# Performance work log

Hardware: AMD Instinct MI355X
Metric: run time of the kernel (lower is better)

Reference implementation:

```python
import jax, jax.numpy as jnp
import numpy as np

EPS = 1e-5


def _conv1x1(w, x):
    # w: [O, C, 1, 1], x: [B, C, H, W] -> [B, O, H, W]
    return jnp.einsum('oc,bchw->bohw', w[:, :, 0, 0], x)


def _bn_train(y, g, b):
    # BatchNorm2d in training mode: batch statistics over (B, H, W)
    m = y.mean(axis=(0, 2, 3), keepdims=True)
    v = y.var(axis=(0, 2, 3), keepdims=True)
    return (y - m) * jax.lax.rsqrt(v + EPS) * g[None, :, None, None] + b[None, :, None, None]


def setup_inputs() -> dict:
    key = jax.random.key(0)
    ks = jax.random.split(key, 8)
    B, C, H, W = 16, 512, 32, 32
    width, heads, hd, out_ch = 128, 4, 32, 512  # out_chans*expansion = 512
    return {
        'x': jax.random.normal(ks[0], (B, C, H, W), jnp.float32),
        'conv1_w': jax.random.normal(ks[1], (width, C, 1, 1), jnp.float32) * 0.05,
        'bn1_g': jnp.ones((width,), jnp.float32),
        'bn1_b': jnp.zeros((width,), jnp.float32),
        'qkv_w': jax.random.normal(ks[2], (3 * width, width, 1, 1), jnp.float32) * 0.05,
        'rw': jax.random.normal(ks[3], (1, heads, hd, 1, W), jnp.float32),
        'rh': jax.random.normal(ks[4], (1, heads, hd, H, 1), jnp.float32),
        'conv2_w': jax.random.normal(ks[5], (out_ch, width, 1, 1), jnp.float32) * 0.05,
        'bn2_g': jnp.ones((out_ch,), jnp.float32),
        'bn2_b': jnp.zeros((out_ch,), jnp.float32),
    }


def reference(x, conv1_w, bn1_g, bn1_b, qkv_w, rw, rh, conv2_w, bn2_g, bn2_b):
    B, C, H, W = x.shape
    heads = rw.shape[1]
    width = qkv_w.shape[1]
    hd = width // heads
    scale = hd ** (-0.5)
    N = H * W

    identity = x
    # conv1 = BaseConv: 1x1 conv (no bias) + BN + ReLU
    y = jax.nn.relu(_bn_train(_conv1x1(conv1_w, x), bn1_g, bn1_b))

    # Attention with relative position bias
    qkv = _conv1x1(qkv_w, y)                       # [B, 3*width, H, W]
    qkv = qkv.reshape(B, 3, heads, hd, N)          # split channels as (3, heads, hd)
    q, k, v = qkv[:, 0], qkv[:, 1], qkv[:, 2]      # each [B, heads, hd, N]

    attn_content = jnp.einsum('bhdn,bhdm->bhnm', q, k) * scale  # [B, heads, N, N]
    r = (rw + rh).reshape(heads, hd, N)                          # [heads, hd, N]
    attn_position = jnp.einsum('bhdn,hdm->bhnm', q, r) * scale
    attn = jax.nn.softmax(attn_content + attn_position, axis=-1)
    out = jnp.einsum('bhnm,bhdm->bhdn', attn, v)   # [B, heads, hd, N]
    y = out.reshape(B, width, H, W)

    # conv2 + BN, residual add, ReLU (stride==1: no pooling, no down_sample)
    y = _bn_train(_conv1x1(conv2_w, y), bn2_g, bn2_b)
    y = y + identity
    return jax.nn.relu(y)
```

## Files before the change

### kernel.cpp

```cpp
#include <hip/hip_runtime.h>
#include <cstddef>
#include <cstdint>

constexpr int BATCH = 16;
constexpr int NQ    = 1024;
constexpr float QSCALE = 0.17677669529663687f * 1.4426950408889634f;

typedef __attribute__((ext_vector_type(8))) short bf8;
typedef __attribute__((ext_vector_type(4))) float f32x4;
typedef __attribute__((ext_vector_type(4))) unsigned short us4;
typedef __attribute__((ext_vector_type(8))) unsigned short us8;

__device__ inline unsigned short f2bf(float x) {
  union { float f; uint32_t u; } c{x};
  uint32_t r = c.u + 0x7fffu + ((c.u >> 16) & 1u);
  return (unsigned short)(r >> 16);
}
__device__ inline float b2f(unsigned short v) {
  union { uint32_t u; float f; } c{(uint32_t)v << 16};
  return c.f;
}
__device__ inline float fast_exp2(float x) {
#if __has_builtin(__builtin_amdgcn_exp2f)
  return __builtin_amdgcn_exp2f(x);
#else
  return exp2f(x);
#endif
}

__global__ __launch_bounds__(256) void k_wcvt(const float* __restrict__ w1,
                                              const float* __restrict__ wq,
                                              const float* __restrict__ w2,
                                              unsigned short* __restrict__ o1,
                                              unsigned short* __restrict__ oq,
                                              unsigned short* __restrict__ o2,
                                              float* __restrict__ S2,
                                              float* __restrict__ Q2) {
  if (blockIdx.x == 88) {
    const int t = threadIdx.x;
    S2[t * 2] = 0.f; S2[t * 2 + 1] = 0.f;
    Q2[t * 2] = 0.f; Q2[t * 2 + 1] = 0.f;
    return;
  }
  int idx = (blockIdx.x * 256 + threadIdx.x) * 8;
  const float* s; unsigned short* d; int off;
  if (idx < 65536)        { s = w1; d = o1; off = idx; }
  else if (idx < 114688)  { s = wq; d = oq; off = idx - 65536; }
  else                    { s = w2; d = o2; off = idx - 114688; }
  float4 a = *(const float4*)(s + off);
  float4 b = *(const float4*)(s + off + 4);
  us8 o = {f2bf(a.x), f2bf(a.y), f2bf(a.z), f2bf(a.w),
           f2bf(b.x), f2bf(b.y), f2bf(b.z), f2bf(b.w)};
  *(us8*)(d + off) = o;
}

__global__ __launch_bounds__(256) void k_conv1(const float* __restrict__ x,
                                               const unsigned short* __restrict__ W,
                                               unsigned short* __restrict__ y1T) {
  constexpr int BS = 68;
  __shared__ unsigned short Bl[64 * BS];

  const int bb = blockIdx.z;
  const int n0 = blockIdx.x * 64;
  const int tid = threadIdx.x, lane = tid & 63, wv = tid >> 6;
  const int wn = wv & 1, wm = wv >> 1;
  const int i = lane & 15, g = lane >> 4;

  const int kb = tid >> 4, nb = tid & 15;

  f32x4 acc[2][4];
#pragma unroll
  for (int a = 0; a < 2; ++a)
#pragma unroll
    for (int b = 0; b < 4; ++b) acc[a][b] = {0.f, 0.f, 0.f, 0.f};

  float4 rv[4];
#pragma unroll
  for (int r = 0; r < 4; ++r)
    rv[r] = *(const float4*)(x + (((size_t)(bb * 512 + kb * 4 + r)) << 10) + n0 + nb * 4);

  for (int s = 0; s < 8; ++s) {
    bf8 wf[4][2];
#pragma unroll
    for (int b = 0; b < 4; ++b)
#pragma unroll
      for (int h = 0; h < 2; ++h)
        wf[b][h] = *(const bf8*)(W + (size_t)(wm * 64 + b * 16 + i) * 512 + s * 64 + h * 32 + g * 8);

    __syncthreads();
#pragma unroll
    for (int j = 0; j < 4; ++j) {
      us4 pk = {f2bf((&rv[0].x)[j]), f2bf((&rv[1].x)[j]),
                f2bf((&rv[2].x)[j]), f2bf((&rv[3].x)[j])};
      *(us4*)&Bl[(nb * 4 + j) * BS + kb * 4] = pk;
    }
    __syncthreads();

    if (s < 7) {
#pragma unroll
      for (int r = 0; r < 4; ++r)
        rv[r] = *(const float4*)(x + (((size_t)(bb * 512 + (s + 1) * 64 + kb * 4 + r)) << 10) + n0 + nb * 4);
    }

#pragma unroll
    for (int h = 0; h < 2; ++h) {
      bf8 af[2];
#pragma unroll
      for (int a = 0; a < 2; ++a)
        af[a] = *(const bf8*)&Bl[(wn * 32 + a * 16 + i) * BS + h * 32 + g * 8];
#pragma unroll
      for (int a = 0; a < 2; ++a)
#pragma unroll
        for (int b = 0; b < 4; ++b)
          acc[a][b] = __builtin_amdgcn_mfma_f32_16x16x32_bf16(wf[b][h], af[a], acc[a][b], 0, 0, 0);
    }
  }

#pragma unroll
  for (int a = 0; a < 2; ++a)
#pragma unroll
    for (int b = 0; b < 4; ++b) {
      const int n = n0 + wn * 32 + a * 16 + i;
      const int c = wm * 64 + b * 16 + 4 * g;
      us4 pk = {f2bf(acc[a][b][0]), f2bf(acc[a][b][1]), f2bf(acc[a][b][2]), f2bf(acc[a][b][3])};
      *(us4*)(y1T + ((size_t)(bb << 10) + n) * 128 + c) = pk;
    }
}

template<int KTOT, int MODE>
__global__ __launch_bounds__(256) void k_mm(const unsigned short* __restrict__ W,
                                            const unsigned short* __restrict__ Bact,
                                            const float* __restrict__ scl,
                                            const float* __restrict__ sht,
                                            const float* __restrict__ rw,
                                            const float* __restrict__ rh,
                                            unsigned short* __restrict__ out0,
                                            unsigned short* __restrict__ out1,
                                            unsigned short* __restrict__ out2) {
  constexpr int BS = 136;
  __shared__ unsigned short Blds[128 * BS];
  __shared__ float scl_s[128], sht_s[128];

  const int bb = blockIdx.z, mt = blockIdx.y;
  const int n0 = blockIdx.x * 128, m0 = mt * 64;
  const int tid = threadIdx.x, lane = tid & 63, wv = tid >> 6;
  const int wn = wv & 1, wm = wv >> 1;
  const int i = lane & 15, g = lane >> 4;

  const unsigned short* Bp = Bact + ((size_t)bb * NQ + n0) * KTOT;

  f32x4 acc[4][2];
#pragma unroll
  for (int a = 0; a < 4; ++a)
#pragma unroll
    for (int b = 0; b < 2; ++b) acc[a][b] = {0.f, 0.f, 0.f, 0.f};

  const int sn = tid >> 1;
  const int sk = (tid & 1) * 8;

  if (tid < 128) { scl_s[tid] = scl[tid]; sht_s[tid] = sht[tid]; }
  bf8 wf[2][4];
#pragma unroll
  for (int b = 0; b < 2; ++b)
#pragma unroll
    for (int h = 0; h < 4; ++h)
      wf[b][h] = *(const bf8*)(W + (size_t)(m0 + wm * 32 + b * 16 + i) * 128 + h * 32 + g * 8);
  __syncthreads();
#pragma unroll
  for (int p = 0; p < 8; ++p) {
    us8 v = *(const us8*)(Bp + (size_t)sn * 128 + sk + p * 16);
    const int kb = sk + p * 16;
    float scv[8], shv[8];
    *(float4*)scv = *(const float4*)&scl_s[kb];
    *(float4*)(scv + 4) = *(const float4*)&scl_s[kb + 4];
    *(float4*)shv = *(const float4*)&sht_s[kb];
    *(float4*)(shv + 4) = *(const float4*)&sht_s[kb + 4];
#pragma unroll
    for (int j = 0; j < 8; ++j)
      v[j] = f2bf(fmaxf(fmaf(b2f(v[j]), scv[j], shv[j]), 0.f));
    *(us8*)(&Blds[sn * BS + sk + p * 16]) = v;
  }
  __syncthreads();

  const bool actA = (mt >= 4);
  if (actA) {
#pragma unroll
    for (int h = 0; h < 4; ++h) {
      bf8 af[4];
#pragma unroll
      for (int a = 0; a < 4; ++a)
        af[a] = *(const bf8*)&Blds[(wn * 64 + a * 16 + i) * BS + h * 32 + g * 8];
#pragma unroll
      for (int a = 0; a < 4; ++a)
#pragma unroll
        for (int b = 0; b < 2; ++b)
          acc[a][b] = __builtin_amdgcn_mfma_f32_16x16x32_bf16(af[a], wf[b][h], acc[a][b], 0, 0, 0);
    }
  } else {
#pragma unroll
    for (int h = 0; h < 4; ++h) {
      bf8 af[4];
#pragma unroll
      for (int a = 0; a < 4; ++a)
        af[a] = *(const bf8*)&Blds[(wn * 64 + a * 16 + i) * BS + h * 32 + g * 8];
#pragma unroll
      for (int a = 0; a < 4; ++a)
#pragma unroll
        for (int b = 0; b < 2; ++b)
          acc[a][b] = __builtin_amdgcn_mfma_f32_16x16x32_bf16(wf[b][h], af[a], acc[a][b], 0, 0, 0);
    }
  }

  if (mt < 2) {
#pragma unroll
    for (int a = 0; a < 4; ++a)
#pragma unroll
      for (int b = 0; b < 2; ++b) {
        const int n = n0 + wn * 64 + a * 16 + i;
        const int c = m0 + wm * 32 + b * 16 + 4 * g;
        const int hh = c >> 5, d = c & 31;
        us4 pk = {f2bf(acc[a][b][0] * QSCALE), f2bf(acc[a][b][1] * QSCALE),
                  f2bf(acc[a][b][2] * QSCALE), f2bf(acc[a][b][3] * QSCALE)};
        *(us4*)(out0 + (((size_t)(bb * 4 + hh) << 10) + n) * 32 + d) = pk;
      }
  } else if (mt < 4) {
#pragma unroll
    for (int a = 0; a < 4; ++a)
#pragma unroll
      for (int b = 0; b < 2; ++b) {
        const int n = n0 + wn * 64 + a * 16 + i;
        const int c = (m0 - 128) + wm * 32 + b * 16 + 4 * g;
        const int hh = c >> 5, d = c & 31;
        const int wcol = n & 31, hrow = n >> 5;
        float vv[4];
#pragma unroll
        for (int r = 0; r < 4; ++r)
          vv[r] = acc[a][b][r] + rw[(c + r) * 32 + wcol] + rh[(c + r) * 32 + hrow];
        us4 pk = {f2bf(vv[0]), f2bf(vv[1]), f2bf(vv[2]), f2bf(vv[3])};
        *(us4*)(out1 + (((size_t)(bb * 4 + hh) << 10) + n) * 32 + d) = pk;
      }
  } else {
#pragma unroll
    for (int a = 0; a < 4; ++a)
#pragma unroll
      for (int b = 0; b < 2; ++b) {
        const int c = (m0 - 256) + wm * 32 + b * 16 + i;
        const int nb = n0 + wn * 64 + a * 16 + 4 * g;
        const int hh = c >> 5, dd = c & 31;
        us4 pk = {f2bf(acc[a][b][0]), f2bf(acc[a][b][1]), f2bf(acc[a][b][2]), f2bf(acc[a][b][3])};
        *(us4*)(out2 + (((size_t)(bb * 4 + hh) * 32 + dd) << 10) + nb) = pk;
      }
  }
}

__global__ __launch_bounds__(256) void k_mm2(const unsigned short* __restrict__ W,
                                             const float* __restrict__ Aof,
                                             float* __restrict__ y2,
                                             float* __restrict__ S2,
                                             float* __restrict__ Q2) {
  constexpr int BS = 264;
  __shared__ unsigned short Blds[64 * BS];
  const int bb = blockIdx.z;
  const int n0 = blockIdx.x * 64;
  const int tid = threadIdx.x, lane = tid & 63, wv = tid >> 6;
  const int wn = wv & 1, wm = wv >> 1;
  const int i = lane & 15, g = lane >> 4;

  const int sn = tid >> 2, sk = (tid & 3) * 32;
  const float* src = Aof + (((size_t)(bb << 10)) + n0 + sn) * 128 + sk;
#pragma unroll
  for (int p = 0; p < 4; ++p) {
    float4 f0 = *(const float4*)(src + p * 8);
    float4 f1 = *(const float4*)(src + p * 8 + 4);
    float fv[8] = {f0.x, f0.y, f0.z, f0.w, f1.x, f1.y, f1.z, f1.w};
    us8 hi, lo;
#pragma unroll
    for (int j = 0; j < 8; ++j) {
      unsigned short h16 = f2bf(fv[j]);
      hi[j] = h16;
      lo[j] = f2bf(fv[j] - b2f(h16));
    }
    *(us8*)&Blds[sn * BS + sk + p * 8]       = hi;
    *(us8*)&Blds[sn * BS + 128 + sk + p * 8] = lo;
  }
  __syncthreads();

  auto loadw = [&](bf8 (&wf)[2][4], int mt) {
#pragma unroll
    for (int b = 0; b < 2; ++b)
#pragma unroll
      for (int h = 0; h < 4; ++h)
        wf[b][h] = *(const bf8*)(W + (size_t)(mt * 64 + wm * 32 + b * 16 + i) * 128 + h * 32 + g * 8);
  };

  auto step = [&](bf8 (&wf)[2][4], int mt) {
    f32x4 acc[2][2];
#pragma unroll
    for (int a = 0; a < 2; ++a)
#pragma unroll
      for (int b = 0; b < 2; ++b) acc[a][b] = {0.f, 0.f, 0.f, 0.f};
#pragma unroll
    for (int h = 0; h < 4; ++h) {
      bf8 ah[2], al[2];
#pragma unroll
      for (int a = 0; a < 2; ++a) {
        ah[a] = *(const bf8*)&Blds[(wn * 32 + a * 16 + i) * BS + h * 32 + g * 8];
        al[a] = *(const bf8*)&Blds[(wn * 32 + a * 16 + i) * BS + 128 + h * 32 + g * 8];
      }
#pragma unroll
      for (int a = 0; a < 2; ++a)
#pragma unroll
        for (int b = 0; b < 2; ++b) {
          acc[a][b] = __builtin_amdgcn_mfma_f32_16x16x32_bf16(ah[a], wf[b][h], acc[a][b], 0, 0, 0);
          acc[a][b] = __builtin_amdgcn_mfma_f32_16x16x32_bf16(al[a], wf[b][h], acc[a][b], 0, 0, 0);
        }
    }
#pragma unroll
    for (int a = 0; a < 2; ++a)
#pragma unroll
      for (int b = 0; b < 2; ++b) {
        const int c = mt * 64 + wm * 32 + b * 16 + i;
        const int nb = n0 + wn * 32 + a * 16 + 4 * g;
        *(f32x4*)(y2 + (((size_t)(bb * 512 + c)) << 10) + nb) = acc[a][b];
      }
#pragma unroll
    for (int b = 0; b < 2; ++b) {
      float s = 0.f, q = 0.f;
#pragma unroll
      for (int a = 0; a < 2; ++a)
#pragma unroll
        for (int r = 0; r < 4; ++r) {
          float v = acc[a][b][r];
          s += v; q += v * v;
        }
      s += __shfl_xor(s, 16); s += __shfl_xor(s, 32);
      q += __shfl_xor(q, 16); q += __shfl_xor(q, 32);
      if (lane < 16) {
        const int c = mt * 64 + wm * 32 + b * 16 + i;
        atomicAdd(&S2[c], s);
        atomicAdd(&Q2[c], q);
      }
    }
  };

  bf8 wfA[2][4], wfB[2][4];
  loadw(wfA, 0);
#pragma unroll
  for (int mp = 0; mp < 4; ++mp) {
    loadw(wfB, 2 * mp + 1);
    step(wfA, 2 * mp);
    if (mp < 3) loadw(wfA, 2 * mp + 2);
    step(wfB, 2 * mp + 1);
  }
}

__global__ __launch_bounds__(256) void k_bnstat1a(const unsigned short* __restrict__ y1T,
                                                  float* __restrict__ pS,
                                                  float* __restrict__ pQ) {
  const int blk = blockIdx.x, t = threadIdx.x;
  const int rr = t >> 4, co = t & 15;
  float s[8], q[8];
#pragma unroll
  for (int j = 0; j < 8; ++j) { s[j] = 0.f; q[j] = 0.f; }
  for (int it = 0; it < 16; ++it) {
    const int r = blk * 256 + rr + it * 16;
    us8 v = *(const us8*)(y1T + (size_t)r * 128 + co * 8);
#pragma unroll
    for (int j = 0; j < 8; ++j) { float f = b2f(v[j]); s[j] += f; q[j] += f * f; }
  }
  __shared__ float rs[16][16][8], rq[16][16][8];
#pragma unroll
  for (int j = 0; j < 8; ++j) { rs[rr][co][j] = s[j]; rq[rr][co][j] = q[j]; }
  __syncthreads();
  if (t < 128) {
    const int c = t;
    float S = 0.f, Q = 0.f;
    for (int r2 = 0; r2 < 16; ++r2) { S += rs[r2][c >> 3][c & 7]; Q += rq[r2][c >> 3][c & 7]; }
    pS[c * 64 + blk] = S;
    pQ[c * 64 + blk] = Q;
  }
}

__global__ __launch_bounds__(128) void k_bnfin1(const float* __restrict__ pS,
                                                const float* __restrict__ pQ,
                                                const float* __restrict__ g,
                                                const float* __restrict__ be,
                                                float* __restrict__ scl,
                                                float* __restrict__ sht) {
  const int c = threadIdx.x;
  float S = 0.f, Q = 0.f;
  for (int k = 0; k < 64; ++k) { S += pS[c * 64 + k]; Q += pQ[c * 64 + k]; }
  const float inv_n = 1.f / 16384.f;
  const float mean = S * inv_n, var = Q * inv_n - mean * mean;
  const float sc = rsqrtf(var + 1e-5f) * g[c];
  scl[c] = sc;
  sht[c] = be[c] - mean * sc;
}

__global__ __launch_bounds__(512) void k_bnfin2(const float* __restrict__ S2,
                                                const float* __restrict__ Q2,
                                                const float* __restrict__ g,
                                                const float* __restrict__ be,
                                                float* __restrict__ scl,
                                                float* __restrict__ sht) {
  const int c = threadIdx.x;
  const float inv_n = 1.f / 16384.f;
  const float mean = S2[c] * inv_n, var = Q2[c] * inv_n - mean * mean;
  const float sc = rsqrtf(var + 1e-5f) * g[c];
  scl[c] = sc;
  sht[c] = be[c] - mean * sc;
}

__global__ __launch_bounds__(256) void k_attn_mfma(const unsigned short* __restrict__ qs,
                                                   const unsigned short* __restrict__ kt,
                                                   const unsigned short* __restrict__ vt,
                                                   float* __restrict__ aoT) {
  const int bh   = blockIdx.y;
  const int tid  = threadIdx.x;
  const int lane = tid & 63;
  const int wv   = tid >> 6;
  const int i    = lane & 15;
  const int g    = lane >> 4;
  const int n0w  = blockIdx.x * 64 + wv * 16;

  __shared__ unsigned short Ks[64 * 56];
  __shared__ unsigned short Vt[32 * 72];

  const bf8 qf = *reinterpret_cast<const bf8*>(
      qs + ((size_t)bh * NQ + n0w + i) * 32 + g * 8);

  f32x4 o0 = {0.f, 0.f, 0.f, 0.f}, o1 = {0.f, 0.f, 0.f, 0.f};
  float m = -1e30f, lsum = 0.f;

  const unsigned short* kb = kt + (size_t)bh * NQ * 32;
  const unsigned short* vb = vt + (size_t)bh * 32 * NQ;

  const int skey = tid >> 2, sds = (tid & 3) * 8;
  const int svd  = tid >> 3, svn = (tid & 7) * 8;

  for (int k0 = 0; k0 < NQ; k0 += 64) {
    bf8 kvld = *reinterpret_cast<const bf8*>(kb + (size_t)(k0 + skey) * 32 + sds);
    bf8 vvld = *reinterpret_cast<const bf8*>(vb + (size_t)svd * NQ + k0 + svn);
    __syncthreads();
    *reinterpret_cast<bf8*>(&Ks[skey * 56 + sds]) = kvld;
    *reinterpret_cast<bf8*>(&Vt[svd * 72 + svn])  = vvld;
    __syncthreads();

    f32x4 st[4];
    const f32x4 zero = {0.f, 0.f, 0.f, 0.f};
#pragma unroll
    for (int t = 0; t < 4; ++t) {
      bf8 kf = *reinterpret_cast<const bf8*>(&Ks[(t * 16 + i) * 56 + g * 8]);
      st[t] = __builtin_amdgcn_mfma_f32_16x16x32_bf16(kf, qf, zero, 0, 0, 0);
    }

    float tmax = st[0][0];
#pragma unroll
    for (int t = 0; t < 4; ++t)
#pragma unroll
      for (int r = 0; r < 4; ++r) tmax = fmaxf(tmax, st[t][r]);
    tmax = fmaxf(tmax, __shfl_xor(tmax, 16));
    tmax = fmaxf(tmax, __shfl_xor(tmax, 32));

    const float mn   = fmaxf(m, tmax);
    const float corr = fast_exp2(m - mn);
    m = mn;

    float ps = 0.f;
    unsigned int pk[4][2];
#pragma unroll
    for (int t = 0; t < 4; ++t) {
      float p0 = fast_exp2(st[t][0] - mn);
      float p1 = fast_exp2(st[t][1] - mn);
      float p2 = fast_exp2(st[t][2] - mn);
      float p3 = fast_exp2(st[t][3] - mn);
      ps += (p0 + p1) + (p2 + p3);
      unsigned int pa, pb;
      asm("v_cvt_pk_bf16_f32 %0, %1, %2" : "=v"(pa) : "v"(p0), "v"(p1));
      asm("v_cvt_pk_bf16_f32 %0, %1, %2" : "=v"(pb) : "v"(p2), "v"(p3));
      pk[t][0] = pa; pk[t][1] = pb;
    }
    ps += __shfl_xor(ps, 16);
    ps += __shfl_xor(ps, 32);
    lsum = lsum * corr + ps;
#pragma unroll
    for (int r = 0; r < 4; ++r) { o0[r] *= corr; o1[r] *= corr; }

    const int src0 = ((g & 1) << 5) + i;
    const int src1 = src0 + 16;
    const bool hi = (g >= 2);
#pragma unroll
    for (int s = 0; s < 2; ++s) {
      int a0 = __shfl((int)pk[2 * s][0], src0);
      int a1 = __shfl((int)pk[2 * s][1], src0);
      int a2 = __shfl((int)pk[2 * s][0], src1);
      int a3 = __shfl((int)pk[2 * s][1], src1);
      int b0 = __shfl((int)pk[2 * s + 1][0], src0);
      int b1 = __shfl((int)pk[2 * s + 1][1], src0);
      int b2 = __shfl((int)pk[2 * s + 1][0], src1);
      int b3 = __shfl((int)pk[2 * s + 1][1], src1);
      union { int d[4]; bf8 v; } pf;
      pf.d[0] = hi ? b0 : a0;
      pf.d[1] = hi ? b1 : a1;
      pf.d[2] = hi ? b2 : a2;
      pf.d[3] = hi ? b3 : a3;
      bf8 vf0 = *reinterpret_cast<const bf8*>(&Vt[(i)      * 72 + s * 32 + g * 8]);
      bf8 vf1 = *reinterpret_cast<const bf8*>(&Vt[(16 + i) * 72 + s * 32 + g * 8]);
      o0 = __builtin_amdgcn_mfma_f32_16x16x32_bf16(vf0, pf.v, o0, 0, 0, 0);
      o1 = __builtin_amdgcn_mfma_f32_16x16x32_bf16(vf1, pf.v, o1, 0, 0, 0);
    }
  }

  const float inv = 1.f / lsum;
  float* dst = aoT + (((size_t)(bh >> 2) << 10) + n0w + i) * 128 + (bh & 3) * 32 + 4 * g;
  f32x4 p0 = {o0[0] * inv, o0[1] * inv, o0[2] * inv, o0[3] * inv};
  f32x4 p1 = {o1[0] * inv, o1[1] * inv, o1[2] * inv, o1[3] * inv};
  *(f32x4*)dst        = p0;
  *(f32x4*)(dst + 16) = p1;
}

__global__ __launch_bounds__(256) void k_final(const float* __restrict__ y2,
                                               const float* __restrict__ x,
                                               const float* __restrict__ scl,
                                               const float* __restrict__ sht,
                                               float* __restrict__ out) {
  const size_t idx = ((size_t)blockIdx.x * 256 + threadIdx.x) * 8;
  const int c = (int)((idx >> 10) & 511);
  const float sc = scl[c], sh = sht[c];
  float4 v0 = *(const float4*)(y2 + idx);
  float4 v1 = *(const float4*)(y2 + idx + 4);
  float4 x0 = *(const float4*)(x + idx);
  float4 x1 = *(const float4*)(x + idx + 4);
  float4 o0, o1;
  o0.x = fmaxf(v0.x * sc + sh + x0.x, 0.f);
  o0.y = fmaxf(v0.y * sc + sh + x0.y, 0.f);
  o0.z = fmaxf(v0.z * sc + sh + x0.z, 0.f);
  o0.w = fmaxf(v0.w * sc + sh + x0.w, 0.f);
  o1.x = fmaxf(v1.x * sc + sh + x1.x, 0.f);
  o1.y = fmaxf(v1.y * sc + sh + x1.y, 0.f);
  o1.z = fmaxf(v1.z * sc + sh + x1.z, 0.f);
  o1.w = fmaxf(v1.w * sc + sh + x1.w, 0.f);
  *(float4*)(out + idx)     = o0;
  *(float4*)(out + idx + 4) = o1;
}

extern "C" void kernel_launch(void* const* d_in, const int* in_sizes, int n_in,
                              void* d_out, int out_size, void* d_ws, size_t ws_size,
                              hipStream_t stream) {
  (void)in_sizes; (void)n_in; (void)out_size; (void)ws_size;
  const float* x    = (const float*)d_in[0];
  const float* w1   = (const float*)d_in[1];
  const float* g1   = (const float*)d_in[2];
  const float* b1   = (const float*)d_in[3];
  const float* wqkv = (const float*)d_in[4];
  const float* rw   = (const float*)d_in[5];
  const float* rh   = (const float*)d_in[6];
  const float* w2   = (const float*)d_in[7];
  const float* g2   = (const float*)d_in[8];
  const float* b2   = (const float*)d_in[9];
  float* out = (float*)d_out;
  char* base = (char*)d_ws;

  float*          y2  = (float*)(base);
  unsigned short* y1T = (unsigned short*)(base + (32u << 20));
  unsigned short* qs  = (unsigned short*)(base + (36u << 20));
  unsigned short* kt  = (unsigned short*)(base + (40u << 20));
  unsigned short* vt  = (unsigned short*)(base + (44u << 20));
  float*          aoT = (float*)(base + (48u << 20));
  unsigned short* wb1 = (unsigned short*)(base + (56u << 20));
  unsigned short* wbq = wb1 + 65536;
  unsigned short* wb2 = wbq + 49152;
  float* pS   = (float*)(base + (57u << 20));
  float* pQ   = pS + 8192;
  float* S2   = pQ + 8192;
  float* Q2   = S2 + 512;
  float* scl1 = Q2 + 512;
  float* sht1 = scl1 + 128;
  float* scl2 = sht1 + 128;
  float* sht2 = scl2 + 512;

  k_wcvt<<<89, 256, 0, stream>>>(w1, wqkv, w2, wb1, wbq, wb2, S2, Q2);
  k_conv1<<<dim3(16, 1, BATCH), 256, 0, stream>>>(x, wb1, y1T);
  k_bnstat1a<<<64, 256, 0, stream>>>(y1T, pS, pQ);
  k_bnfin1<<<1, 128, 0, stream>>>(pS, pQ, g1, b1, scl1, sht1);
  k_mm<128, 1><<<dim3(8, 6, BATCH), 256, 0, stream>>>(wbq, y1T, scl1, sht1,
                                                      rw, rh, qs, kt, vt);
  k_attn_mfma<<<dim3(NQ / 64, BATCH * 4), 256, 0, stream>>>(qs, kt, vt, aoT);
  k_mm2<<<dim3(16, 1, BATCH), 256, 0, stream>>>(wb2, aoT, y2, S2, Q2);
  k_bnfin2<<<1, 512, 0, stream>>>(S2, Q2, g2, b2, scl2, sht2);
  k_final<<<4096, 256, 0, stream>>>(y2, x, scl2, sht2, out);
}
```

Before: 124.9 us.

## Split conv2 GEMM over output halves and replace global BN atomics with partials

k_mm2 now launches twice as many blocks, each covering half of the 512 output channels, which doubles grid parallelism at the cost of loading and splitting the activation tile into bf16 hi/lo twice. BN2 statistics are first gathered in shared memory with LDS atomics and written as per-block partials, rather than issued as global float atomics. A new k_bnfin2 reduces 256 partials per channel using a 64-thread block per channel. This removes global atomic contention and the zero-init of the accumulators in k_wcvt.

```diff
diff --git a/kernel.cpp b/kernel.cpp
--- a/kernel.cpp
+++ b/kernel.cpp
@@ -33,15 +33,7 @@
                                               const float* __restrict__ w2,
                                               unsigned short* __restrict__ o1,
                                               unsigned short* __restrict__ oq,
-                                              unsigned short* __restrict__ o2,
-                                              float* __restrict__ S2,
-                                              float* __restrict__ Q2) {
-  if (blockIdx.x == 88) {
-    const int t = threadIdx.x;
-    S2[t * 2] = 0.f; S2[t * 2 + 1] = 0.f;
-    Q2[t * 2] = 0.f; Q2[t * 2 + 1] = 0.f;
-    return;
-  }
+                                              unsigned short* __restrict__ o2) {
   int idx = (blockIdx.x * 256 + threadIdx.x) * 8;
   const float* s; unsigned short* d; int off;
   if (idx < 65536)        { s = w1; d = o1; off = idx; }
@@ -256,15 +248,19 @@
 __global__ __launch_bounds__(256) void k_mm2(const unsigned short* __restrict__ W,
                                              const float* __restrict__ Aof,
                                              float* __restrict__ y2,
-                                             float* __restrict__ S2,
-                                             float* __restrict__ Q2) {
+                                             float* __restrict__ pBS,
+                                             float* __restrict__ pBQ) {
   constexpr int BS = 264;
   __shared__ unsigned short Blds[64 * BS];
+  __shared__ float Sl[256], Ql[256];
   const int bb = blockIdx.z;
+  const int mh = blockIdx.y;
   const int n0 = blockIdx.x * 64;
   const int tid = threadIdx.x, lane = tid & 63, wv = tid >> 6;
   const int wn = wv & 1, wm = wv >> 1;
   const int i = lane & 15, g = lane >> 4;
+
+  Sl[tid] = 0.f; Ql[tid] = 0.f;
 
   const int sn = tid >> 2, sk = (tid & 3) * 32;
   const float* src = Aof + (((size_t)(bb << 10)) + n0 + sn) * 128 + sk;
@@ -285,7 +281,8 @@
   }
   __syncthreads();
 
-  auto loadw = [&](bf8 (&wf)[2][4], int mt) {
+  auto loadw = [&](bf8 (&wf)[2][4], int lp) {
+    const int mt = mh * 4 + lp;
 #pragma unroll
     for (int b = 0; b < 2; ++b)
 #pragma unroll
@@ -293,7 +290,8 @@
         wf[b][h] = *(const bf8*)(W + (size_t)(mt * 64 + wm * 32 + b * 16 + i) * 128 + h * 32 + g * 8);
   };
 
-  auto step = [&](bf8 (&wf)[2][4], int mt) {
+  auto step = [&](bf8 (&wf)[2][4], int lp) {
+    const int mt = mh * 4 + lp;
     f32x4 acc[2][2];
 #pragma unroll
     for (int a = 0; a < 2; ++a)
@@ -335,10 +333,10 @@
         }
       s += __shfl_xor(s, 16); s += __shfl_xor(s, 32);
       q += __shfl_xor(q, 16); q += __shfl_xor(q, 32);
-      if (lane < 16) {
-        const int c = mt * 64 + wm * 32 + b * 16 + i;
-        atomicAdd(&S2[c], s);
-        atomicAdd(&Q2[c], q);
+      if ((lane & 48) == 0) {
+        const int cl = lp * 64 + wm * 32 + b * 16 + i;
+        atomicAdd(&Sl[cl], s);
+        atomicAdd(&Ql[cl], q);
       }
     }
   };
@@ -346,12 +344,17 @@
   bf8 wfA[2][4], wfB[2][4];
   loadw(wfA, 0);
 #pragma unroll
-  for (int mp = 0; mp < 4; ++mp) {
+  for (int mp = 0; mp < 2; ++mp) {
     loadw(wfB, 2 * mp + 1);
     step(wfA, 2 * mp);
-    if (mp < 3) loadw(wfA, 2 * mp + 2);
+    if (mp < 1) loadw(wfA, 2 * mp + 2);
     step(wfB, 2 * mp + 1);
   }
+
+  __syncthreads();
+  const int pidx = bb * 16 + blockIdx.x;
+  pBS[(size_t)(mh * 256 + tid) * 256 + pidx] = Sl[tid];
+  pBQ[(size_t)(mh * 256 + tid) * 256 + pidx] = Ql[tid];
 }
 
 __global__ __launch_bounds__(256) void k_bnstat1a(const unsigned short* __restrict__ y1T,
@@ -397,18 +400,31 @@
   sht[c] = be[c] - mean * sc;
 }
 
-__global__ __launch_bounds__(512) void k_bnfin2(const float* __restrict__ S2,
-                                                const float* __restrict__ Q2,
-                                                const float* __restrict__ g,
-                                                const float* __restrict__ be,
-                                                float* __restrict__ scl,
-                                                float* __restrict__ sht) {
-  const int c = threadIdx.x;
-  const float inv_n = 1.f / 16384.f;
-  const float mean = S2[c] * inv_n, var = Q2[c] * inv_n - mean * mean;
-  const float sc = rsqrtf(var + 1e-5f) * g[c];
-  scl[c] = sc;
-  sht[c] = be[c] - mean * sc;
+__global__ __launch_bounds__(64) void k_bnfin2(const float* __restrict__ pBS,
+                                               const float* __restrict__ pBQ,
+                                               const float* __restrict__ g,
+                                               const float* __restrict__ be,
+                                               float* __restrict__ scl,
+                                               float* __restrict__ sht) {
+  const int c = blockIdx.x, t = threadIdx.x;
+  float S = 0.f, Q = 0.f;
+#pragma unroll
+  for (int k = 0; k < 4; ++k) {
+    S += pBS[(size_t)c * 256 + t + k * 64];
+    Q += pBQ[(size_t)c * 256 + t + k * 64];
+  }
+#pragma unroll
+  for (int o = 32; o > 0; o >>= 1) {
+    S += __shfl_down(S, o);
+    Q += __shfl_down(Q, o);
+  }
+  if (t == 0) {
+    const float inv_n = 1.f / 16384.f;
+    const float mean = S * inv_n, var = Q * inv_n - mean * mean;
+    const float sc = rsqrtf(var + 1e-5f) * g[c];
+    scl[c] = sc;
+    sht[c] = be[c] - mean * sc;
+  }
 }
 
 __global__ __launch_bounds__(256) void k_attn_mfma(const unsigned short* __restrict__ qs,
@@ -572,21 +588,21 @@
   unsigned short* wb2 = wbq + 49152;
   float* pS   = (float*)(base + (57u << 20));
   float* pQ   = pS + 8192;
-  float* S2   = pQ + 8192;
-  float* Q2   = S2 + 512;
-  float* scl1 = Q2 + 512;
+  float* pBS  = pQ + 8192;
+  float* pBQ  = pBS + 131072;
+  float* scl1 = pBQ + 131072;
   float* sht1 = scl1 + 128;
   float* scl2 = sht1 + 128;
   float* sht2 = scl2 + 512;
 
-  k_wcvt<<<89, 256, 0, stream>>>(w1, wqkv, w2, wb1, wbq, wb2, S2, Q2);
+  k_wcvt<<<88, 256, 0, stream>>>(w1, wqkv, w2, wb1, wbq, wb2);
   k_conv1<<<dim3(16, 1, BATCH), 256, 0, stream>>>(x, wb1, y1T);
   k_bnstat1a<<<64, 256, 0, stream>>>(y1T, pS, pQ);
   k_bnfin1<<<1, 128, 0, stream>>>(pS, pQ, g1, b1, scl1, sht1);
   k_mm<128, 1><<<dim3(8, 6, BATCH), 256, 0, stream>>>(wbq, y1T, scl1, sht1,
                                                       rw, rh, qs, kt, vt);
   k_attn_mfma<<<dim3(NQ / 64, BATCH * 4), 256, 0, stream>>>(qs, kt, vt, aoT);
-  k_mm2<<<dim3(16, 1, BATCH), 256, 0, stream>>>(wb2, aoT, y2, S2, Q2);
-  k_bnfin2<<<1, 512, 0, stream>>>(S2, Q2, g2, b2, scl2, sht2);
+  k_mm2<<<dim3(16, 2, BATCH), 256, 0, stream>>>(wb2, aoT, y2, pBS, pBQ);
+  k_bnfin2<<<512, 64, 0, stream>>>(pBS, pBQ, g2, b2, scl2, sht2);
   k_final<<<4096, 256, 0, stream>>>(y2, x, scl2, sht2, out);
 }
```

After: 111.5 us. -10.7%, faster.
